# Kernel optimization log

Measured on AMD Instinct MI355X. Metric: run time of the kernel, lower is better.

Reference implementation:

```python
import jax, jax.numpy as jnp
import numpy as np

B, T, C = 256, 1024, 128


def setup_inputs() -> dict:
    key = jax.random.key(0)
    k1, k2 = jax.random.split(key)
    potentials = jax.random.normal(k1, (B, T, C), dtype=jnp.float32)
    # glorot_uniform init for the [C, C] transition matrix
    limit = float(np.sqrt(6.0 / (C + C)))
    transitions = jax.random.uniform(k2, (C, C), minval=-limit, maxval=limit, dtype=jnp.float32)
    return {"potentials": potentials, "transitions": transitions}


def _viterbi_decode(potentials, transitions):
    """Equivalent of tfa.text.crf.crf_decode with full sequence lengths ('reg' mode).

    potentials: [B, T, C] unary scores; transitions: [C, C] (prev -> cur).
    Returns one-hot decoded tags [B, T, C] (the layer's inference output).
    """
    num_tags = potentials.shape[-1]
    pots_t = jnp.swapaxes(potentials, 0, 1)  # [T, B, C]
    alpha0 = pots_t[0]                        # [B, C]

    def fwd_step(alpha, pot):
        # max-plus DP step: scores[b, p, c] = alpha[b, p] + transitions[p, c]
        scores = alpha[:, :, None] + transitions[None, :, :]   # [B, C, C]
        bp = jnp.argmax(scores, axis=1).astype(jnp.int32)      # backpointers [B, C]
        alpha_new = jnp.max(scores, axis=1) + pot               # [B, C]
        return alpha_new, bp

    alpha_T, bps = jax.lax.scan(fwd_step, alpha0, pots_t[1:])   # bps: [T-1, B, C]
    last_tag = jnp.argmax(alpha_T, axis=-1).astype(jnp.int32)   # [B]

    def bwd_step(tag, bp):
        # tag at time t+1 -> best tag at time t via backpointers
        prev = jnp.take_along_axis(bp, tag[:, None], axis=1)[:, 0]
        return prev, prev

    _, prev_tags = jax.lax.scan(bwd_step, last_tag, bps, reverse=True)  # [T-1, B]
    tags = jnp.concatenate([prev_tags, last_tag[None, :]], axis=0)      # [T, B]
    tags = jnp.swapaxes(tags, 0, 1)                                      # [B, T]
    return jax.nn.one_hot(tags, num_tags, dtype=potentials.dtype)


def reference(potentials, transitions):
    return _viterbi_decode(potentials, transitions)
```

## Files before the change

kernel.cpp:

```cpp
#include <hip/hip_runtime.h>


typedef float f32x2 __attribute__((ext_vector_type(2)));
typedef unsigned int u32x4 __attribute__((ext_vector_type(4)));

constexpr int NB = 256;
constexpr int NT = 1024;
constexpr int NC = 128;

template <int CTRL>
__device__ __forceinline__ float fmax_dpp(float v) {
  int x = __builtin_amdgcn_update_dpp(__float_as_int(v), __float_as_int(v),
                                      CTRL, 0xF, 0xF, false);
  return fmaxf(v, __int_as_float(x));
}
__device__ __forceinline__ float wave_max_to_lane63(float m) {
  m = fmax_dpp<0x111>(m);
  m = fmax_dpp<0x112>(m);
  m = fmax_dpp<0x114>(m);
  m = fmax_dpp<0x118>(m);
  m = fmax_dpp<0x142>(m);
  m = fmax_dpp<0x143>(m);
  return m;
}

constexpr int ABUF = 192;

#define DPP2(CTL)                                                          \
  "v_max_f32_dpp v32, v32, v32 " CTL " row_mask:0xf bank_mask:0xf\n\t"     \
  "v_max_f32_dpp v96, v96, v96 " CTL " row_mask:0xf bank_mask:0xf\n\t"

#define STEP_S(RD, WR, PC, SOFF)                                           \
  "ds_read_b128 v[48:51], %[" RD "]\n\t"                                   \
  "ds_read_b128 v[52:55], %[" RD "] offset:16\n\t"                         \
  "ds_read_b128 v[56:59], %[" RD "] offset:48\n\t"                         \
  "ds_read_b128 v[60:63], %[" RD "] offset:64\n\t"                         \
  "s_waitcnt lgkmcnt(2)\n\t"                                               \
  "v_pk_add_f32 v[32:33], v[48:49], v[64:65]\n\t"                          \
  "v_pk_add_f32 v[96:97], v[48:49], v[80:81]\n\t"                          \
  "v_pk_add_f32 v[34:35], v[50:51], v[66:67]\n\t"                          \
  "v_pk_add_f32 v[98:99], v[50:51], v[82:83]\n\t"                          \
  "v_pk_add_f32 v[36:37], v[52:53], v[68:69]\n\t"                          \
  "v_pk_add_f32 v[100:101], v[52:53], v[84:85]\n\t"                        \
  "v_pk_add_f32 v[38:39], v[54:55], v[70:71]\n\t"                          \
  "v_pk_add_f32 v[102:103], v[54:55], v[86:87]\n\t"                        \
  "v_max3_f32 v32, v32, v33, v34\n\t"                                      \
  "v_max3_f32 v96, v96, v97, v98\n\t"                                      \
  "v_max3_f32 v35, v35, v36, v37\n\t"                                      \
  "v_max3_f32 v99, v99, v100, v101\n\t"                                    \
  "s_waitcnt lgkmcnt(0)\n\t"                                               \
  "v_pk_add_f32 v[40:41], v[56:57], v[72:73]\n\t"                          \
  "v_pk_add_f32 v[104:105], v[56:57], v[88:89]\n\t"                        \
  "v_pk_add_f32 v[42:43], v[58:59], v[74:75]\n\t"                          \
  "v_pk_add_f32 v[106:107], v[58:59], v[90:91]\n\t"                        \
  "v_pk_add_f32 v[44:45], v[60:61], v[76:77]\n\t"                          \
  "v_pk_add_f32 v[108:109], v[60:61], v[92:93]\n\t"                        \
  "v_pk_add_f32 v[46:47], v[62:63], v[78:79]\n\t"                          \
  "v_pk_add_f32 v[110:111], v[62:63], v[94:95]\n\t"                        \
  "v_max3_f32 v38, v38, v39, v40\n\t"                                      \
  "v_max3_f32 v102, v102, v103, v104\n\t"                                  \
  "v_max3_f32 v41, v41, v42, v43\n\t"                                      \
  "v_max3_f32 v105, v105, v106, v107\n\t"                                  \
  "v_max3_f32 v44, v44, v45, v46\n\t"                                      \
  "v_max3_f32 v108, v108, v109, v110\n\t"                                  \
  "v_max3_f32 v32, v32, v35, v38\n\t"                                      \
  "v_max3_f32 v96, v96, v99, v102\n\t"                                     \
  "v_max3_f32 v41, v41, v44, v47\n\t"                                      \
  "v_max3_f32 v105, v105, v108, v111\n\t"                                  \
  "v_max_f32 v32, v32, v41\n\t"                                            \
  "v_max_f32 v96, v96, v105\n\t"                                           \
  "s_nop 1\n\t"                                                            \
  DPP2("quad_perm:[1,0,3,2]")                                              \
  "s_nop 0\n\t"                                                            \
  DPP2("quad_perm:[2,3,0,1]")                                              \
  "s_nop 0\n\t"                                                            \
  DPP2("row_half_mirror")                                                  \
  "s_nop 0\n\t"                                                            \
  "v_cndmask_b32 v41, v32, v96, %[selb0]\n\t"                              \
  "s_mov_b64 exec, %[wmask]\n\t"                                           \
  "v_add_f32 v40, v41, %[" PC "]\n\t"                                      \
  "ds_write_b32 %[" WR "], v40\n\t"                                        \
  "global_store_dword %[qoff], v41, %[sout] offset:" SOFF "\n\t"           \
  "s_mov_b64 exec, -1\n\t"                                                 \
  "s_waitcnt lgkmcnt(0)\n\t"                                               \
  "s_barrier\n\t"

#define LDT(R, B, O) "global_load_dword v" R ", %[" B "], %[strans] offset:" O "\n\t"

__global__ __launch_bounds__(512)
void crf_fused(const float* __restrict__ pot, const float* __restrict__ trans,
               float* __restrict__ out) {
  extern __shared__ __align__(16) float smem[];
  float* alpha = smem;
  float* tTf = smem + 2 * ABUF;

  const int tid = threadIdx.x;
  const int b = blockIdx.x;
  const int w = tid >> 6;
  const int l = tid & 63;
  const int g = l >> 3;
  const int i = l & 7;
  const int G = w * 8 + g;
  const bool wr = (l & 7) < 2;
  const int cw = 16 * w + 2 * g + (l & 1);
  const int widx = 12 * (cw >> 3) + (cw & 7);

  const float* potb = pot + (size_t)b * NT * NC;
  float* outb = out + (size_t)b * NT * NC;

  unsigned rda = (unsigned)(size_t)(alpha + 24 * i);
  unsigned rdb = (unsigned)(size_t)(alpha + ABUF + 24 * i);
  unsigned wra = (unsigned)(size_t)(alpha + widx);
  unsigned wrb = (unsigned)(size_t)(alpha + ABUF + widx);

  unsigned toff  = (unsigned)((16 * i * NC + 2 * G) * 4);
  unsigned toff2 = toff + 4096;
  unsigned qoff = (unsigned)((1 * NC + cw) * 4);
  unsigned poff = ((unsigned)b * (NT * NC) + 5 * NC + cw) * 4u;
  unsigned long long strans = (unsigned long long)(size_t)trans;
  unsigned long long sout = (unsigned long long)(size_t)outb;
  unsigned long long pbase = (unsigned long long)(size_t)pot;
  u32x4 srd;
  srd.x = (unsigned)pbase;
  srd.y = (unsigned)(pbase >> 32) & 0xFFFFu;
  srd.z = (unsigned)(NB * NT * NC) * 4u;
  srd.w = 0x00020000u;
  unsigned long long selb0 = 0xAAAAAAAAAAAAAAAAull;
  unsigned long long wmask = 0x0303030303030303ull;
  int cnt = 254;

  float pc0 = potb[1 * NC + cw], pc1 = potb[2 * NC + cw];
  float pc2 = potb[3 * NC + cw], pc3 = potb[4 * NC + cw];
  float pn0 = 0.f, pn1 = 0.f, pn2 = 0.f, pn3 = 0.f;

  if (wr) {
    alpha[widx] = potb[cw];
    outb[cw] = 0.0f;
  }
  __syncthreads();

  asm volatile(
      LDT("64","toff","0")     LDT("65","toff","512")
      LDT("66","toff","1024")  LDT("67","toff","1536")
      LDT("68","toff","2048")  LDT("69","toff","2560")
      LDT("70","toff","3072")  LDT("71","toff","3584")
      LDT("72","toff2","0")    LDT("73","toff2","512")
      LDT("74","toff2","1024") LDT("75","toff2","1536")
      LDT("76","toff2","2048") LDT("77","toff2","2560")
      LDT("78","toff2","3072") LDT("79","toff2","3584")
      LDT("80","toff","4")     LDT("81","toff","516")
      LDT("82","toff","1028")  LDT("83","toff","1540")
      LDT("84","toff","2052")  LDT("85","toff","2564")
      LDT("86","toff","3076")  LDT("87","toff","3588")
      LDT("88","toff2","4")    LDT("89","toff2","516")
      LDT("90","toff2","1028") LDT("91","toff2","1540")
      LDT("92","toff2","2052") LDT("93","toff2","2564")
      LDT("94","toff2","3076") LDT("95","toff2","3588")
      "s_waitcnt vmcnt(0)\n\t"
      "buffer_load_dword %[pn0], %[poff], %[srd], 0 offen\n\t"
      "buffer_load_dword %[pn1], %[poff], %[srd], 0 offen offset:512\n\t"
      "buffer_load_dword %[pn2], %[poff], %[srd], 0 offen offset:1024\n\t"
      "buffer_load_dword %[pn3], %[poff], %[srd], 0 offen offset:1536\n\t"
      "L_crfmain_%=:\n\t"
      STEP_S("rda", "wrb", "pc0", "0")
      STEP_S("rdb", "wra", "pc1", "512")
      STEP_S("rda", "wrb", "pc2", "1024")
      STEP_S("rdb", "wra", "pc3", "1536")
      "s_waitcnt vmcnt(4)\n\t"
      "v_mov_b32 %[pc0], %[pn0]\n\t"
      "v_mov_b32 %[pc1], %[pn1]\n\t"
      "v_mov_b32 %[pc2], %[pn2]\n\t"
      "v_mov_b32 %[pc3], %[pn3]\n\t"
      "v_add_u32 %[poff], 0x800, %[poff]\n\t"
      "v_add_u32 %[qoff], 0x800, %[qoff]\n\t"
      "buffer_load_dword %[pn0], %[poff], %[srd], 0 offen\n\t"
      "buffer_load_dword %[pn1], %[poff], %[srd], 0 offen offset:512\n\t"
      "buffer_load_dword %[pn2], %[poff], %[srd], 0 offen offset:1024\n\t"
      "buffer_load_dword %[pn3], %[poff], %[srd], 0 offen offset:1536\n\t"
      "s_sub_u32 %[cnt], %[cnt], 1\n\t"
      "s_cmp_lg_u32 %[cnt], 0\n\t"
      "s_cbranch_scc1 L_crfmain_%=\n\t"
      STEP_S("rda", "wrb", "pc0", "0")
      STEP_S("rdb", "wra", "pc1", "512")
      STEP_S("rda", "wrb", "pc2", "1024")
      STEP_S("rdb", "wra", "pc3", "1536")
      "s_waitcnt vmcnt(4)\n\t"
      "v_mov_b32 %[pc0], %[pn0]\n\t"
      "v_mov_b32 %[pc1], %[pn1]\n\t"
      "v_mov_b32 %[pc2], %[pn2]\n\t"
      "v_add_u32 %[qoff], 0x800, %[qoff]\n\t"
      STEP_S("rda", "wrb", "pc0", "0")
      STEP_S("rdb", "wra", "pc1", "512")
      STEP_S("rda", "wrb", "pc2", "1024")
      "s_waitcnt vmcnt(0)\n\t"
      : [pc0] "+v"(pc0), [pc1] "+v"(pc1), [pc2] "+v"(pc2), [pc3] "+v"(pc3),
        [pn0] "+v"(pn0), [pn1] "+v"(pn1), [pn2] "+v"(pn2), [pn3] "+v"(pn3),
        [qoff] "+v"(qoff), [poff] "+v"(poff), [cnt] "+s"(cnt)
      : [toff] "v"(toff), [toff2] "v"(toff2),
        [rda] "v"(rda), [rdb] "v"(rdb), [wra] "v"(wra), [wrb] "v"(wrb),
        [strans] "s"(strans), [sout] "s"(sout), [srd] "s"(srd),
        [selb0] "s"(selb0), [wmask] "s"(wmask)
      : "memory", "scc",
        "v32", "v33", "v34", "v35", "v36", "v37", "v38", "v39",
        "v40", "v41", "v42", "v43", "v44", "v45", "v46", "v47",
        "v48", "v49", "v50", "v51", "v52", "v53", "v54", "v55",
        "v56", "v57", "v58", "v59", "v60", "v61", "v62", "v63",
        "v64", "v65", "v66", "v67", "v68", "v69", "v70", "v71",
        "v72", "v73", "v74", "v75", "v76", "v77", "v78", "v79",
        "v80", "v81", "v82", "v83", "v84", "v85", "v86", "v87",
        "v88", "v89", "v90", "v91", "v92", "v93", "v94", "v95",
        "v96", "v97", "v98", "v99", "v100", "v101", "v102", "v103",
        "v104", "v105", "v106", "v107", "v108", "v109", "v110", "v111");

  __syncthreads();
  {
    const int rr = tid >> 2;
    const int q4 = tid & 3;
    const float4* src = (const float4*)(trans + rr * NC + q4 * 32);
    const int lo = rr & 63, hb = rr >> 6;
    #pragma unroll
    for (int j = 0; j < 8; ++j) {
      float4 qv = src[j];
      int cb = q4 * 32 + 4 * j;
      tTf[(cb + 0) * 128 + lo * 2 + hb] = qv.x;
      tTf[(cb + 1) * 128 + lo * 2 + hb] = qv.y;
      tTf[(cb + 2) * 128 + lo * 2 + hb] = qv.z;
      tTf[(cb + 3) * 128 + lo * 2 + hb] = qv.w;
    }
  }
  __syncthreads();
  if (tid >= 64) return;
  const f32x2* tTp = (const f32x2*)tTf;

  float qlo_t = outb[(NT - 1) * NC + l];
  float qhi_t = outb[(NT - 1) * NC + 64 + l];
  float alo_t = qlo_t + potb[(NT - 1) * NC + l];
  float ahi_t = qhi_t + potb[(NT - 1) * NC + 64 + l];
  float m0 = wave_max_to_lane63(fmaxf(alo_t, ahi_t));
  float M0 = __int_as_float(__builtin_amdgcn_readlane(__float_as_int(m0), 63));
  unsigned long long bl = __ballot(alo_t == M0);
  unsigned long long bh = __ballot(ahi_t == M0);
  int tag = bl ? (__ffsll((long long)bl) - 1)
               : (64 + __ffsll((long long)bh) - 1);

  float cqlo[8], cqhi[8], calo[8], cahi[8];
  float nqlo[8], nqhi[8], nplo[8], nphi[8];
  #pragma unroll
  for (int j = 0; j < 8; ++j) {
    int rw = NT - 2 - j;
    cqlo[j] = outb[rw * NC + l];
    cqhi[j] = outb[rw * NC + 64 + l];
    calo[j] = cqlo[j] + potb[rw * NC + l];
    cahi[j] = cqhi[j] + potb[rw * NC + 64 + l];
  }

  for (int g2 = 0; g2 < 128; ++g2) {
    #pragma unroll
    for (int j = 0; j < 8; ++j) {
      int rw = NT - 10 - 8 * g2 - j;
      if (rw < 0) rw = 0;
      nqlo[j] = outb[rw * NC + l];
      nqhi[j] = outb[rw * NC + 64 + l];
      nplo[j] = potb[rw * NC + l];
      nphi[j] = potb[rw * NC + 64 + l];
    }
    #pragma unroll
    for (int j = 0; j < 8; ++j) {
      int t = NT - 1 - 8 * g2 - j;
      if (t >= 1) {
        outb[t * NC + l]      = (l == tag) ? 1.0f : 0.0f;
        outb[t * NC + 64 + l] = (64 + l == tag) ? 1.0f : 0.0f;
        int Mlo = __builtin_amdgcn_readlane(__float_as_int(qlo_t), tag & 63);
        int Mhi = __builtin_amdgcn_readlane(__float_as_int(qhi_t), tag & 63);
        float M = __int_as_float((tag < 64) ? Mlo : Mhi);
        f32x2 tt = tTp[tag * 64 + l];
        float vlo = calo[j] + tt.x;
        float vhi = cahi[j] + tt.y;
        unsigned long long el = __ballot(vlo == M);
        unsigned long long eh = __ballot(vhi == M);
        tag = el ? (__ffsll((long long)el) - 1)
                 : (64 + __ffsll((long long)eh) - 1);
        qlo_t = cqlo[j];
        qhi_t = cqhi[j];
      }
    }
    #pragma unroll
    for (int j = 0; j < 8; ++j) {
      cqlo[j] = nqlo[j]; cqhi[j] = nqhi[j];
      calo[j] = nqlo[j] + nplo[j];
      cahi[j] = nqhi[j] + nphi[j];
    }
  }
  outb[l]      = (l == tag) ? 1.0f : 0.0f;
  outb[64 + l] = (64 + l == tag) ? 1.0f : 0.0f;
}


extern "C" void kernel_launch(void* const* d_in, const int* in_sizes, int n_in,
                              void* d_out, int out_size, void* d_ws, size_t ws_size,
                              hipStream_t stream) {
  const float* pot   = (const float*)d_in[0];
  const float* trans = (const float*)d_in[1];
  float* out = (float*)d_out;

  constexpr int SMEM = (2 * ABUF + NC * NC) * 4;
  hipFuncSetAttribute((const void*)crf_fused,
                      hipFuncAttributeMaxDynamicSharedMemorySize, SMEM);

  crf_fused<<<NB, 512, SMEM, stream>>>(pot, trans, out);
}
```

Before: 414.2 us.

## Double workgroup to 1024 threads and halve per-lane reduction work in Viterbi step

Moves the forward max-plus recurrence from 512 to 1024 threads per batch row. Each 16-lane group now reduces over 8 predecessors per lane for two tags at once, adding a row_mirror DPP stage, and writes alpha and backpointer-max pairs with 64-bit stores. Potentials are prefetched two chunks ahead as dwordx2 loads. The goal is to shorten the serial per-timestep latency with fewer LDS reads and adds per lane, at the cost of more waves meeting at each barrier and higher register-pressure limits from the launch bounds.

```diff
diff --git a/kernel.cpp b/kernel.cpp
--- a/kernel.cpp
+++ b/kernel.cpp
@@ -26,68 +26,50 @@
 
 constexpr int ABUF = 192;
 
-#define DPP2(CTL)                                                          \
-  "v_max_f32_dpp v32, v32, v32 " CTL " row_mask:0xf bank_mask:0xf\n\t"     \
-  "v_max_f32_dpp v96, v96, v96 " CTL " row_mask:0xf bank_mask:0xf\n\t"
-
-#define STEP_S(RD, WR, PC, SOFF)                                           \
+#define DPPR2(CTL)                                                         \
+  "v_max_f32_dpp v56, v56, v56 " CTL " row_mask:0xf bank_mask:0xf\n\t"     \
+  "v_max_f32_dpp v57, v57, v57 " CTL " row_mask:0xf bank_mask:0xf\n\t"
+
+#define STEP_S(RD, WR, PCP, SOFF)                                          \
   "ds_read_b128 v[48:51], %[" RD "]\n\t"                                   \
   "ds_read_b128 v[52:55], %[" RD "] offset:16\n\t"                         \
-  "ds_read_b128 v[56:59], %[" RD "] offset:48\n\t"                         \
-  "ds_read_b128 v[60:63], %[" RD "] offset:64\n\t"                         \
-  "s_waitcnt lgkmcnt(2)\n\t"                                               \
+  "s_waitcnt lgkmcnt(0)\n\t"                                               \
   "v_pk_add_f32 v[32:33], v[48:49], v[64:65]\n\t"                          \
-  "v_pk_add_f32 v[96:97], v[48:49], v[80:81]\n\t"                          \
+  "v_pk_add_f32 v[40:41], v[48:49], v[72:73]\n\t"                          \
   "v_pk_add_f32 v[34:35], v[50:51], v[66:67]\n\t"                          \
-  "v_pk_add_f32 v[98:99], v[50:51], v[82:83]\n\t"                          \
+  "v_pk_add_f32 v[42:43], v[50:51], v[74:75]\n\t"                          \
   "v_pk_add_f32 v[36:37], v[52:53], v[68:69]\n\t"                          \
-  "v_pk_add_f32 v[100:101], v[52:53], v[84:85]\n\t"                        \
+  "v_pk_add_f32 v[44:45], v[52:53], v[76:77]\n\t"                          \
   "v_pk_add_f32 v[38:39], v[54:55], v[70:71]\n\t"                          \
-  "v_pk_add_f32 v[102:103], v[54:55], v[86:87]\n\t"                        \
-  "v_max3_f32 v32, v32, v33, v34\n\t"                                      \
-  "v_max3_f32 v96, v96, v97, v98\n\t"                                      \
+  "v_pk_add_f32 v[46:47], v[54:55], v[78:79]\n\t"                          \
+  "v_max3_f32 v56, v32, v33, v34\n\t"                                      \
+  "v_max3_f32 v57, v40, v41, v42\n\t"                                      \
   "v_max3_f32 v35, v35, v36, v37\n\t"                                      \
-  "v_max3_f32 v99, v99, v100, v101\n\t"                                    \
-  "s_waitcnt lgkmcnt(0)\n\t"                                               \
-  "v_pk_add_f32 v[40:41], v[56:57], v[72:73]\n\t"                          \
-  "v_pk_add_f32 v[104:105], v[56:57], v[88:89]\n\t"                        \
-  "v_pk_add_f32 v[42:43], v[58:59], v[74:75]\n\t"                          \
-  "v_pk_add_f32 v[106:107], v[58:59], v[90:91]\n\t"                        \
-  "v_pk_add_f32 v[44:45], v[60:61], v[76:77]\n\t"                          \
-  "v_pk_add_f32 v[108:109], v[60:61], v[92:93]\n\t"                        \
-  "v_pk_add_f32 v[46:47], v[62:63], v[78:79]\n\t"                          \
-  "v_pk_add_f32 v[110:111], v[62:63], v[94:95]\n\t"                        \
-  "v_max3_f32 v38, v38, v39, v40\n\t"                                      \
-  "v_max3_f32 v102, v102, v103, v104\n\t"                                  \
-  "v_max3_f32 v41, v41, v42, v43\n\t"                                      \
-  "v_max3_f32 v105, v105, v106, v107\n\t"                                  \
-  "v_max3_f32 v44, v44, v45, v46\n\t"                                      \
-  "v_max3_f32 v108, v108, v109, v110\n\t"                                  \
-  "v_max3_f32 v32, v32, v35, v38\n\t"                                      \
-  "v_max3_f32 v96, v96, v99, v102\n\t"                                     \
-  "v_max3_f32 v41, v41, v44, v47\n\t"                                      \
-  "v_max3_f32 v105, v105, v108, v111\n\t"                                  \
-  "v_max_f32 v32, v32, v41\n\t"                                            \
-  "v_max_f32 v96, v96, v105\n\t"                                           \
+  "v_max3_f32 v43, v43, v44, v45\n\t"                                      \
+  "v_max3_f32 v56, v56, v35, v38\n\t"                                      \
+  "v_max3_f32 v57, v57, v43, v46\n\t"                                      \
+  "v_max_f32 v56, v56, v39\n\t"                                            \
+  "v_max_f32 v57, v57, v47\n\t"                                            \
   "s_nop 1\n\t"                                                            \
-  DPP2("quad_perm:[1,0,3,2]")                                              \
-  "s_nop 0\n\t"                                                            \
-  DPP2("quad_perm:[2,3,0,1]")                                              \
-  "s_nop 0\n\t"                                                            \
-  DPP2("row_half_mirror")                                                  \
-  "s_nop 0\n\t"                                                            \
-  "v_cndmask_b32 v41, v32, v96, %[selb0]\n\t"                              \
+  DPPR2("quad_perm:[1,0,3,2]")                                             \
+  "s_nop 0\n\t"                                                            \
+  DPPR2("quad_perm:[2,3,0,1]")                                             \
+  "s_nop 0\n\t"                                                            \
+  DPPR2("row_half_mirror")                                                  \
+  "s_nop 0\n\t"                                                            \
+  DPPR2("row_mirror")                                                      \
+  "s_nop 0\n\t"                                                            \
   "s_mov_b64 exec, %[wmask]\n\t"                                           \
-  "v_add_f32 v40, v41, %[" PC "]\n\t"                                      \
-  "ds_write_b32 %[" WR "], v40\n\t"                                        \
-  "global_store_dword %[qoff], v41, %[sout] offset:" SOFF "\n\t"           \
+  "v_pk_add_f32 v[58:59], v[56:57], v[" PCP "]\n\t"                        \
+  "ds_write_b64 %[" WR "], v[58:59]\n\t"                                   \
+  "global_store_dwordx2 %[qoff], v[56:57], %[sout] offset:" SOFF "\n\t"    \
   "s_mov_b64 exec, -1\n\t"                                                 \
   "s_waitcnt lgkmcnt(0)\n\t"                                               \
   "s_barrier\n\t"
 
-#define LDT(R, B, O) "global_load_dword v" R ", %[" B "], %[strans] offset:" O "\n\t"
-
-__global__ __launch_bounds__(512)
+#define LDT(R, O) "global_load_dword v" R ", %[toff], %[strans] offset:" O "\n\t"
+
+__global__ __launch_bounds__(1024, 4)
 void crf_fused(const float* __restrict__ pot, const float* __restrict__ trans,
                float* __restrict__ out) {
   extern __shared__ __align__(16) float smem[];
@@ -98,25 +80,24 @@
   const int b = blockIdx.x;
   const int w = tid >> 6;
   const int l = tid & 63;
-  const int g = l >> 3;
-  const int i = l & 7;
-  const int G = w * 8 + g;
-  const bool wr = (l & 7) < 2;
-  const int cw = 16 * w + 2 * g + (l & 1);
-  const int widx = 12 * (cw >> 3) + (cw & 7);
+  const int g = l >> 4;
+  const int i = l & 15;
+  const int G = w * 4 + g;
+  const int c0 = 2 * G;
+  const bool wr = (i == 0);
+  const int widx = 12 * (c0 >> 3) + (c0 & 7);
 
   const float* potb = pot + (size_t)b * NT * NC;
   float* outb = out + (size_t)b * NT * NC;
 
-  unsigned rda = (unsigned)(size_t)(alpha + 24 * i);
-  unsigned rdb = (unsigned)(size_t)(alpha + ABUF + 24 * i);
+  unsigned rda = (unsigned)(size_t)(alpha + 12 * i);
+  unsigned rdb = (unsigned)(size_t)(alpha + ABUF + 12 * i);
   unsigned wra = (unsigned)(size_t)(alpha + widx);
   unsigned wrb = (unsigned)(size_t)(alpha + ABUF + widx);
 
-  unsigned toff  = (unsigned)((16 * i * NC + 2 * G) * 4);
-  unsigned toff2 = toff + 4096;
-  unsigned qoff = (unsigned)((1 * NC + cw) * 4);
-  unsigned poff = ((unsigned)b * (NT * NC) + 5 * NC + cw) * 4u;
+  unsigned toff = (unsigned)((8 * i * NC + c0) * 4);
+  unsigned qoff = (unsigned)((1 * NC + c0) * 4);
+  unsigned poff = ((unsigned)b * (NT * NC) + 1 * NC + c0) * 4u;
   unsigned long long strans = (unsigned long long)(size_t)trans;
   unsigned long long sout = (unsigned long long)(size_t)outb;
   unsigned long long pbase = (unsigned long long)(size_t)pot;
@@ -125,103 +106,94 @@
   srd.y = (unsigned)(pbase >> 32) & 0xFFFFu;
   srd.z = (unsigned)(NB * NT * NC) * 4u;
   srd.w = 0x00020000u;
-  unsigned long long selb0 = 0xAAAAAAAAAAAAAAAAull;
-  unsigned long long wmask = 0x0303030303030303ull;
+  unsigned long long wmask = 0x0001000100010001ull;
   int cnt = 254;
 
-  float pc0 = potb[1 * NC + cw], pc1 = potb[2 * NC + cw];
-  float pc2 = potb[3 * NC + cw], pc3 = potb[4 * NC + cw];
-  float pn0 = 0.f, pn1 = 0.f, pn2 = 0.f, pn3 = 0.f;
-
   if (wr) {
-    alpha[widx] = potb[cw];
-    outb[cw] = 0.0f;
+    alpha[widx] = potb[c0];
+    alpha[widx + 1] = potb[c0 + 1];
+    outb[c0] = 0.0f;
+    outb[c0 + 1] = 0.0f;
   }
   __syncthreads();
 
   asm volatile(
-      LDT("64","toff","0")     LDT("65","toff","512")
-      LDT("66","toff","1024")  LDT("67","toff","1536")
-      LDT("68","toff","2048")  LDT("69","toff","2560")
-      LDT("70","toff","3072")  LDT("71","toff","3584")
-      LDT("72","toff2","0")    LDT("73","toff2","512")
-      LDT("74","toff2","1024") LDT("75","toff2","1536")
-      LDT("76","toff2","2048") LDT("77","toff2","2560")
-      LDT("78","toff2","3072") LDT("79","toff2","3584")
-      LDT("80","toff","4")     LDT("81","toff","516")
-      LDT("82","toff","1028")  LDT("83","toff","1540")
-      LDT("84","toff","2052")  LDT("85","toff","2564")
-      LDT("86","toff","3076")  LDT("87","toff","3588")
-      LDT("88","toff2","4")    LDT("89","toff2","516")
-      LDT("90","toff2","1028") LDT("91","toff2","1540")
-      LDT("92","toff2","2052") LDT("93","toff2","2564")
-      LDT("94","toff2","3076") LDT("95","toff2","3588")
-      "s_waitcnt vmcnt(0)\n\t"
-      "buffer_load_dword %[pn0], %[poff], %[srd], 0 offen\n\t"
-      "buffer_load_dword %[pn1], %[poff], %[srd], 0 offen offset:512\n\t"
-      "buffer_load_dword %[pn2], %[poff], %[srd], 0 offen offset:1024\n\t"
-      "buffer_load_dword %[pn3], %[poff], %[srd], 0 offen offset:1536\n\t"
+      LDT("64","0")    LDT("65","512")  LDT("66","1024") LDT("67","1536")
+      LDT("68","2048") LDT("69","2560") LDT("70","3072") LDT("71","3584")
+      LDT("72","4")    LDT("73","516")  LDT("74","1028") LDT("75","1540")
+      LDT("76","2052") LDT("77","2564") LDT("78","3076") LDT("79","3588")
+      "s_mov_b64 exec, %[wmask]\n\t"
+      "buffer_load_dwordx2 v[80:81], %[poff], %[srd], 0 offen\n\t"
+      "buffer_load_dwordx2 v[82:83], %[poff], %[srd], 0 offen offset:512\n\t"
+      "buffer_load_dwordx2 v[84:85], %[poff], %[srd], 0 offen offset:1024\n\t"
+      "buffer_load_dwordx2 v[86:87], %[poff], %[srd], 0 offen offset:1536\n\t"
+      "v_add_u32 %[poff], 0x800, %[poff]\n\t"
+      "buffer_load_dwordx2 v[88:89], %[poff], %[srd], 0 offen\n\t"
+      "buffer_load_dwordx2 v[90:91], %[poff], %[srd], 0 offen offset:512\n\t"
+      "buffer_load_dwordx2 v[92:93], %[poff], %[srd], 0 offen offset:1024\n\t"
+      "buffer_load_dwordx2 v[94:95], %[poff], %[srd], 0 offen offset:1536\n\t"
+      "v_add_u32 %[poff], 0x800, %[poff]\n\t"
+      "s_mov_b64 exec, -1\n\t"
+      "s_waitcnt vmcnt(4)\n\t"
       "L_crfmain_%=:\n\t"
-      STEP_S("rda", "wrb", "pc0", "0")
-      STEP_S("rdb", "wra", "pc1", "512")
-      STEP_S("rda", "wrb", "pc2", "1024")
-      STEP_S("rdb", "wra", "pc3", "1536")
+      STEP_S("rda", "wrb", "80:81", "0")
+      STEP_S("rdb", "wra", "82:83", "512")
+      STEP_S("rda", "wrb", "84:85", "1024")
+      STEP_S("rdb", "wra", "86:87", "1536")
       "s_waitcnt vmcnt(4)\n\t"
-      "v_mov_b32 %[pc0], %[pn0]\n\t"
-      "v_mov_b32 %[pc1], %[pn1]\n\t"
-      "v_mov_b32 %[pc2], %[pn2]\n\t"
-      "v_mov_b32 %[pc3], %[pn3]\n\t"
+      "v_mov_b32 v80, v88\n\t"  "v_mov_b32 v81, v89\n\t"
+      "v_mov_b32 v82, v90\n\t"  "v_mov_b32 v83, v91\n\t"
+      "v_mov_b32 v84, v92\n\t"  "v_mov_b32 v85, v93\n\t"
+      "v_mov_b32 v86, v94\n\t"  "v_mov_b32 v87, v95\n\t"
+      "v_add_u32 %[qoff], 0x800, %[qoff]\n\t"
+      "s_mov_b64 exec, %[wmask]\n\t"
+      "buffer_load_dwordx2 v[88:89], %[poff], %[srd], 0 offen\n\t"
+      "buffer_load_dwordx2 v[90:91], %[poff], %[srd], 0 offen offset:512\n\t"
+      "buffer_load_dwordx2 v[92:93], %[poff], %[srd], 0 offen offset:1024\n\t"
+      "buffer_load_dwordx2 v[94:95], %[poff], %[srd], 0 offen offset:1536\n\t"
+      "s_mov_b64 exec, -1\n\t"
       "v_add_u32 %[poff], 0x800, %[poff]\n\t"
-      "v_add_u32 %[qoff], 0x800, %[qoff]\n\t"
-      "buffer_load_dword %[pn0], %[poff], %[srd], 0 offen\n\t"
-      "buffer_load_dword %[pn1], %[poff], %[srd], 0 offen offset:512\n\t"
-      "buffer_load_dword %[pn2], %[poff], %[srd], 0 offen offset:1024\n\t"
-      "buffer_load_dword %[pn3], %[poff], %[srd], 0 offen offset:1536\n\t"
       "s_sub_u32 %[cnt], %[cnt], 1\n\t"
       "s_cmp_lg_u32 %[cnt], 0\n\t"
       "s_cbranch_scc1 L_crfmain_%=\n\t"
-      STEP_S("rda", "wrb", "pc0", "0")
-      STEP_S("rdb", "wra", "pc1", "512")
-      STEP_S("rda", "wrb", "pc2", "1024")
-      STEP_S("rdb", "wra", "pc3", "1536")
+      STEP_S("rda", "wrb", "80:81", "0")
+      STEP_S("rdb", "wra", "82:83", "512")
+      STEP_S("rda", "wrb", "84:85", "1024")
+      STEP_S("rdb", "wra", "86:87", "1536")
       "s_waitcnt vmcnt(4)\n\t"
-      "v_mov_b32 %[pc0], %[pn0]\n\t"
-      "v_mov_b32 %[pc1], %[pn1]\n\t"
-      "v_mov_b32 %[pc2], %[pn2]\n\t"
+      "v_mov_b32 v80, v88\n\t"  "v_mov_b32 v81, v89\n\t"
+      "v_mov_b32 v82, v90\n\t"  "v_mov_b32 v83, v91\n\t"
+      "v_mov_b32 v84, v92\n\t"  "v_mov_b32 v85, v93\n\t"
       "v_add_u32 %[qoff], 0x800, %[qoff]\n\t"
-      STEP_S("rda", "wrb", "pc0", "0")
-      STEP_S("rdb", "wra", "pc1", "512")
-      STEP_S("rda", "wrb", "pc2", "1024")
+      STEP_S("rda", "wrb", "80:81", "0")
+      STEP_S("rdb", "wra", "82:83", "512")
+      STEP_S("rda", "wrb", "84:85", "1024")
       "s_waitcnt vmcnt(0)\n\t"
-      : [pc0] "+v"(pc0), [pc1] "+v"(pc1), [pc2] "+v"(pc2), [pc3] "+v"(pc3),
-        [pn0] "+v"(pn0), [pn1] "+v"(pn1), [pn2] "+v"(pn2), [pn3] "+v"(pn3),
-        [qoff] "+v"(qoff), [poff] "+v"(poff), [cnt] "+s"(cnt)
-      : [toff] "v"(toff), [toff2] "v"(toff2),
-        [rda] "v"(rda), [rdb] "v"(rdb), [wra] "v"(wra), [wrb] "v"(wrb),
+      : [qoff] "+v"(qoff), [poff] "+v"(poff), [cnt] "+s"(cnt)
+      : [toff] "v"(toff), [rda] "v"(rda), [rdb] "v"(rdb),
+        [wra] "v"(wra), [wrb] "v"(wrb),
         [strans] "s"(strans), [sout] "s"(sout), [srd] "s"(srd),
-        [selb0] "s"(selb0), [wmask] "s"(wmask)
+        [wmask] "s"(wmask)
       : "memory", "scc",
         "v32", "v33", "v34", "v35", "v36", "v37", "v38", "v39",
         "v40", "v41", "v42", "v43", "v44", "v45", "v46", "v47",
         "v48", "v49", "v50", "v51", "v52", "v53", "v54", "v55",
-        "v56", "v57", "v58", "v59", "v60", "v61", "v62", "v63",
+        "v56", "v57", "v58", "v59",
         "v64", "v65", "v66", "v67", "v68", "v69", "v70", "v71",
         "v72", "v73", "v74", "v75", "v76", "v77", "v78", "v79",
         "v80", "v81", "v82", "v83", "v84", "v85", "v86", "v87",
-        "v88", "v89", "v90", "v91", "v92", "v93", "v94", "v95",
-        "v96", "v97", "v98", "v99", "v100", "v101", "v102", "v103",
-        "v104", "v105", "v106", "v107", "v108", "v109", "v110", "v111");
+        "v88", "v89", "v90", "v91", "v92", "v93", "v94", "v95");
 
   __syncthreads();
   {
-    const int rr = tid >> 2;
-    const int q4 = tid & 3;
-    const float4* src = (const float4*)(trans + rr * NC + q4 * 32);
+    const int rr = tid >> 3;
+    const int k8 = tid & 7;
+    const float4* src = (const float4*)(trans + rr * NC) + k8 * 4;
     const int lo = rr & 63, hb = rr >> 6;
     #pragma unroll
-    for (int j = 0; j < 8; ++j) {
+    for (int j = 0; j < 4; ++j) {
       float4 qv = src[j];
-      int cb = q4 * 32 + 4 * j;
+      int cb = (k8 * 4 + j) * 4;
       tTf[(cb + 0) * 128 + lo * 2 + hb] = qv.x;
       tTf[(cb + 1) * 128 + lo * 2 + hb] = qv.y;
       tTf[(cb + 2) * 128 + lo * 2 + hb] = qv.z;
@@ -307,5 +279,5 @@
   hipFuncSetAttribute((const void*)crf_fused,
                       hipFuncAttributeMaxDynamicSharedMemorySize, SMEM);
 
-  crf_fused<<<NB, 512, SMEM, stream>>>(pot, trans, out);
-}
+  crf_fused<<<NB, 1024, SMEM, stream>>>(pot, trans, out);
+}
```

New measurement: 523.1 us. +26.3%, slower.
